# Kernel tuning notes

Hardware: AMD Instinct MI355X
Metric: run time of the kernel (lower is better)

The kernel has to match this reference:

```python
import jax, jax.numpy as jnp
import numpy as np

D, H, W, C = 24, 24, 16, 2        # image_dims + num_classes
THETA_ALPHA = 160.0               # bilateral spatial std
THETA_BETA = 3.0                  # bilateral intensity std
THETA_GAMMA = 3.0                 # spatial-only std
NUM_ITERATIONS = 5
N = D * H * W


def _gauss_kernel(feats):
    # Dense Gaussian kernel K_ij = exp(-0.5 * ||f_i - f_j||^2).
    # This is the exact filter that the permutohedral lattice approximates
    # (self-term included, matching the lattice splat/blur/slice behaviour).
    sq = jnp.sum(feats * feats, axis=-1)               # [N]
    d2 = sq[:, None] + sq[None, :] - 2.0 * feats @ feats.T
    return jnp.exp(-0.5 * jnp.maximum(d2, 0.0))        # [N, N]


def _positions():
    zz, yy, xx = jnp.meshgrid(jnp.arange(D), jnp.arange(H), jnp.arange(W), indexing='ij')
    return jnp.stack([zz, yy, xx], axis=-1).reshape(N, 3).astype(jnp.float32)


def setup_inputs() -> dict:
    key = jax.random.key(0)
    k1, k2 = jax.random.split(key)
    unaries = jax.random.normal(k1, (1, D, H, W, C), dtype=jnp.float32)
    rgb = jax.random.uniform(k2, (1, D, H, W, 1), dtype=jnp.float32)
    # learned params (build() initial values)
    spatial_ker_weights = jnp.array([1.41, 1.41], dtype=jnp.float32)
    bilateral_ker_weights = jnp.array([3.85, 3.85], dtype=jnp.float32)
    compatibility_matrix = jnp.eye(C, dtype=jnp.float32)
    return dict(unaries=unaries, rgb=rgb,
                spatial_ker_weights=spatial_ker_weights,
                bilateral_ker_weights=bilateral_ker_weights,
                compatibility_matrix=compatibility_matrix)


def reference(unaries, rgb, spatial_ker_weights, bilateral_ker_weights, compatibility_matrix):
    out_shape = unaries.shape
    u = unaries.reshape(N, C)                 # batch index 0 only, as in the TF code
    img = rgb.reshape(N, -1)
    pos = _positions()

    Ks = _gauss_kernel(pos / THETA_GAMMA)                                        # spatial kernel [N,N]
    Kb = _gauss_kernel(jnp.concatenate([pos / THETA_ALPHA, img / THETA_BETA], -1))  # bilateral kernel [N,N]

    # normalization = filter applied to all-ones (row sums)
    norm_s = jnp.sum(Ks, axis=-1, keepdims=True)   # [N,1]
    norm_b = jnp.sum(Kb, axis=-1, keepdims=True)   # [N,1]

    q = u
    for _ in range(NUM_ITERATIONS):
        spatial_out = (Ks @ q) / norm_s            # [N,C]
        bilateral_out = (Kb @ q) / norm_b          # [N,C]
        # diag(w_s) @ spatial.T + diag(w_b) @ bilateral.T  ==  per-class scaling
        message = spatial_out * spatial_ker_weights + bilateral_out * bilateral_ker_weights
        pairwise = message @ compatibility_matrix.T  # (compat @ msg.T).T
        q = u - pairwise
    return q.reshape(out_shape)
```

## Files before the change

### kernel.cpp

```cpp
#include <hip/hip_runtime.h>


#define DD 24
#define HH 24
#define WW 16
#define SLICE 384
#define NPTS 9216
#define NT 5
#define NFI 12
#define NFT 17
#define LOG2E 1.4426950408889634f
#define K3L   (LOG2E / 18.0f)
#define K160L (LOG2E / 51200.0f)

static __device__ __forceinline__ int iabs(int a) { return a < 0 ? -a : a; }

__global__ __launch_bounds__(SLICE)
void k_pre(const float2* __restrict__ u2, const float* __restrict__ rgb,
           float* __restrict__ tmp) {
    __shared__ float gk[32];
    __shared__ float sA[HH][WW + 1];
    __shared__ float sB[HH][WW + 1];
    const int z = blockIdx.x, f = blockIdx.y, t = threadIdx.x;
    const int y = t >> 4, x = t & 15;
    const int i = z * SLICE + t;

    const float kk = (f < 2) ? K3L : K160L;
    if (t < DD) gk[t] = exp2f(-(float)(t * t) * kk);

    float v;
    if (f < 2) {
        float2 q = u2[i];
        v = (f == 0) ? q.x : q.y;
    } else {
        float I3 = rgb[i] * (1.f / 3.f);
        float E = exp2f(-0.5f * LOG2E * I3 * I3);
        int k = (f < NFI) ? ((f - 2) >> 1) : (f - NFI);
        float P = E;
        for (int s = 0; s < k; ++s) P *= I3;
        if (f < NFI) {
            float2 q = u2[i];
            v = P * (((f - 2) & 1) ? q.y : q.x);
        } else {
            v = P;
        }
    }
    sA[y][x] = v;
    __syncthreads();

    float a = 0.f;
#pragma unroll
    for (int xp = 0; xp < WW; ++xp) a = fmaf(gk[iabs(x - xp)], sA[y][xp], a);
    sB[y][x] = a;
    __syncthreads();

    float b = 0.f;
#pragma unroll
    for (int yp = 0; yp < HH; ++yp) b = fmaf(gk[iabs(y - yp)], sB[yp][x], b);
    tmp[f * NPTS + i] = b;
}

__global__ __launch_bounds__(SLICE)
void k_zconv(const float* __restrict__ tmp, float* __restrict__ zout) {
    __shared__ float gk[32];
    const int z = blockIdx.x, f = blockIdx.y, t = threadIdx.x;
    const float kk = (f < 2) ? K3L : K160L;
    if (t < DD) gk[t] = exp2f(-(float)(t * t) * kk);
    __syncthreads();

    float acc = 0.f;
    const float* p = tmp + f * NPTS + t;
#pragma unroll 4
    for (int zp = 0; zp < DD; ++zp)
        acc = fmaf(gk[iabs(z - zp)], p[zp * SLICE], acc);
    zout[f * NPTS + z * SLICE + t] = acc;
}

static __device__ __forceinline__ void mf_update(
        const float acc[12], const float* g3s, const float* Pt,
        float inv_nb, int y, int x, int z,
        const float* sw, const float* bw, const float* compat,
        const float2 uu, float* q0o, float* q1o) {
    const float invf[NT] = {1.f, 1.f, 0.5f, 1.f / 6.f, 1.f / 24.f};
    float sx = 0.f, sy = 0.f, sz = 0.f;
#pragma unroll
    for (int xp = 0; xp < WW; ++xp) sx += g3s[iabs(x - xp)];
#pragma unroll
    for (int yp = 0; yp < HH; ++yp) sy += g3s[iabs(y - yp)];
#pragma unroll
    for (int zp = 0; zp < DD; ++zp) sz += g3s[iabs(z - zp)];
    const float inv_ns = 1.0f / (sx * sy * sz);

    float b0 = 0.f, b1 = 0.f;
#pragma unroll
    for (int k = 0; k < NT; ++k) {
        float w = Pt[k] * invf[k];
        b0 = fmaf(w, acc[2 + 2 * k], b0);
        b1 = fmaf(w, acc[3 + 2 * k], b1);
    }
    b0 *= inv_nb;
    b1 *= inv_nb;
    float s0 = acc[0] * inv_ns;
    float s1 = acc[1] * inv_ns;
    float m0 = s0 * sw[0] + b0 * bw[0];
    float m1 = s1 * sw[1] + b1 * bw[1];
    float p0 = fmaf(compat[0], m0, compat[1] * m1);
    float p1 = fmaf(compat[2], m0, compat[3] * m1);
    *q0o = uu.x - p0;
    *q1o = uu.y - p1;
}

__global__ __launch_bounds__(SLICE)
void k_xyupd(const float* __restrict__ zout, const float* __restrict__ rgb,
             const float2* __restrict__ u2,
             const float* __restrict__ sw, const float* __restrict__ bw,
             const float* __restrict__ compat,
             float* __restrict__ normb, float* __restrict__ tmp, int it) {
    __shared__ float g3s[32];
    __shared__ float gk[32];
    __shared__ float sA[HH][WW + 1];
    __shared__ float sB[HH][WW + 1];
    const int z = blockIdx.x, f = blockIdx.y, t = threadIdx.x;
    const int y = t >> 4, x = t & 15;
    const int i = z * SLICE + t;

    if (t < DD) {
        g3s[t] = exp2f(-(float)(t * t) * K3L);
        gk[t] = exp2f(-(float)(t * t) * ((f < 2) ? K3L : K160L));
    }
    __syncthreads();

    float acc[12];
#pragma unroll
    for (int k = 0; k < 12; ++k) acc[k] = zout[k * NPTS + i];

    const float I3 = rgb[i] * (1.f / 3.f);
    const float E = exp2f(-0.5f * LOG2E * I3 * I3);
    float Pt[NT];
    Pt[0] = E;
#pragma unroll
    for (int k = 1; k < NT; ++k) Pt[k] = Pt[k - 1] * I3;

    float inv_nb;
    if (it == 0) {
        const float invf[NT] = {1.f, 1.f, 0.5f, 1.f / 6.f, 1.f / 24.f};
        float nb = 0.f;
#pragma unroll
        for (int k = 0; k < NT; ++k)
            nb = fmaf(Pt[k] * invf[k], zout[(NFI + k) * NPTS + i], nb);
        if (f == 0) normb[i] = nb;
        inv_nb = 1.0f / nb;
    } else {
        inv_nb = 1.0f / normb[i];
    }

    float q0, q1;
    mf_update(acc, g3s, Pt, inv_nb, y, x, z, sw, bw, compat, u2[i], &q0, &q1);

    float v;
    if (f == 0) v = q0;
    else if (f == 1) v = q1;
    else {
        int k = (f - 2) >> 1;
        v = Pt[k] * (((f - 2) & 1) ? q1 : q0);
    }

    sA[y][x] = v;
    __syncthreads();
    float a = 0.f;
#pragma unroll
    for (int xp = 0; xp < WW; ++xp) a = fmaf(gk[iabs(x - xp)], sA[y][xp], a);
    sB[y][x] = a;
    __syncthreads();
    float b = 0.f;
#pragma unroll
    for (int yp = 0; yp < HH; ++yp) b = fmaf(gk[iabs(y - yp)], sB[yp][x], b);
    tmp[f * NPTS + i] = b;
}

__global__ __launch_bounds__(256)
void k_final(const float* __restrict__ zout, const float* __restrict__ rgb,
             const float2* __restrict__ u2,
             const float* __restrict__ sw, const float* __restrict__ bw,
             const float* __restrict__ compat,
             const float* __restrict__ normb, float2* __restrict__ out) {
    __shared__ float g3s[32];
    const int t = threadIdx.x;
    const int i = blockIdx.x * 256 + t;
    if (t < DD) g3s[t] = exp2f(-(float)(t * t) * K3L);
    __syncthreads();

    const int z = i / SLICE;
    const int yx = i - z * SLICE;
    const int y = yx >> 4, x = yx & 15;

    float acc[12];
#pragma unroll
    for (int k = 0; k < 12; ++k) acc[k] = zout[k * NPTS + i];

    const float I3 = rgb[i] * (1.f / 3.f);
    const float E = exp2f(-0.5f * LOG2E * I3 * I3);
    float Pt[NT];
    Pt[0] = E;
#pragma unroll
    for (int k = 1; k < NT; ++k) Pt[k] = Pt[k - 1] * I3;

    float q0, q1;
    mf_update(acc, g3s, Pt, 1.0f / normb[i], y, x, z, sw, bw, compat,
              u2[i], &q0, &q1);
    out[i] = make_float2(q0, q1);
}

extern "C" void kernel_launch(void* const* d_in, const int* in_sizes, int n_in,
                              void* d_out, int out_size, void* d_ws, size_t ws_size,
                              hipStream_t stream) {
    const float2* u2     = (const float2*)d_in[0];
    const float*  rgb    = (const float*)d_in[1];
    const float*  sw     = (const float*)d_in[2];
    const float*  bw     = (const float*)d_in[3];
    const float*  compat = (const float*)d_in[4];
    float2* out = (float2*)d_out;

    float* ws = (float*)d_ws;
    float* tmp   = ws;
    float* zout  = ws + NFT * NPTS;
    float* normb = ws + 2 * NFT * NPTS;

    k_pre<<<dim3(DD, NFT), SLICE, 0, stream>>>(u2, rgb, tmp);

    for (int it = 0; it < 5; ++it) {
        k_zconv<<<dim3(DD, it == 0 ? NFT : NFI), SLICE, 0, stream>>>(tmp, zout);
        if (it < 4)
            k_xyupd<<<dim3(DD, NFI), SLICE, 0, stream>>>(zout, rgb, u2, sw, bw,
                                                         compat, normb, tmp, it);
        else
            k_final<<<NPTS / 256, 256, 0, stream>>>(zout, rgb, u2, sw, bw,
                                                    compat, normb, out);
    }
}
```

Measured before the change: 103.8 us.

## Pack feature channels into float2 pairs and precompute spatial normalization

New measurement: 97.28 us (median of 2 runs). 6.3% less time.

```diff
diff --git a/kernel.cpp b/kernel.cpp
--- a/kernel.cpp
+++ b/kernel.cpp
@@ -7,101 +7,113 @@
 #define SLICE 384
 #define NPTS 9216
 #define NT 5
-#define NFI 12
-#define NFT 17
+#define NPAIR 6
+#define NPTOT 9
 #define LOG2E 1.4426950408889634f
 #define K3L   (LOG2E / 18.0f)
 #define K160L (LOG2E / 51200.0f)
+#define EXP2  __builtin_amdgcn_exp2f
 
 static __device__ __forceinline__ int iabs(int a) { return a < 0 ? -a : a; }
 
 __global__ __launch_bounds__(SLICE)
 void k_pre(const float2* __restrict__ u2, const float* __restrict__ rgb,
-           float* __restrict__ tmp) {
+           float2* __restrict__ tmp2, float* __restrict__ normS) {
     __shared__ float gk[32];
-    __shared__ float sA[HH][WW + 1];
-    __shared__ float sB[HH][WW + 1];
-    const int z = blockIdx.x, f = blockIdx.y, t = threadIdx.x;
+    __shared__ float2 sA[HH][WW + 1];
+    __shared__ float2 sB[HH][WW + 1];
+    const int z = blockIdx.x, p = blockIdx.y, t = threadIdx.x;
     const int y = t >> 4, x = t & 15;
     const int i = z * SLICE + t;
 
-    const float kk = (f < 2) ? K3L : K160L;
-    if (t < DD) gk[t] = exp2f(-(float)(t * t) * kk);
-
-    float v;
-    if (f < 2) {
+    const float kk = (p == 0) ? K3L : K160L;
+    if (t < DD) gk[t] = EXP2(-(float)(t * t) * kk);
+
+    const float I3 = rgb[i] * (1.f / 3.f);
+    float Pt[NT];
+    Pt[0] = EXP2(-0.5f * LOG2E * I3 * I3);
+#pragma unroll
+    for (int k = 1; k < NT; ++k) Pt[k] = Pt[k - 1] * I3;
+
+    float2 v;
+    if (p == 0) {
+        v = u2[i];
+    } else if (p < NPAIR) {
         float2 q = u2[i];
-        v = (f == 0) ? q.x : q.y;
+        float P = Pt[p - 1];
+        v = make_float2(P * q.x, P * q.y);
     } else {
-        float I3 = rgb[i] * (1.f / 3.f);
-        float E = exp2f(-0.5f * LOG2E * I3 * I3);
-        int k = (f < NFI) ? ((f - 2) >> 1) : (f - NFI);
-        float P = E;
-        for (int s = 0; s < k; ++s) P *= I3;
-        if (f < NFI) {
-            float2 q = u2[i];
-            v = P * (((f - 2) & 1) ? q.y : q.x);
-        } else {
-            v = P;
-        }
+        int j = p - NPAIR;
+        v = make_float2(Pt[2 * j], (j < 2) ? Pt[2 * j + 1] : 0.f);
     }
     sA[y][x] = v;
     __syncthreads();
 
-    float a = 0.f;
-#pragma unroll
-    for (int xp = 0; xp < WW; ++xp) a = fmaf(gk[iabs(x - xp)], sA[y][xp], a);
-    sB[y][x] = a;
-    __syncthreads();
-
-    float b = 0.f;
-#pragma unroll
-    for (int yp = 0; yp < HH; ++yp) b = fmaf(gk[iabs(y - yp)], sB[yp][x], b);
-    tmp[f * NPTS + i] = b;
+    float a0 = 0.f, a1 = 0.f;
+#pragma unroll
+    for (int xp = 0; xp < WW; ++xp) {
+        float w = gk[iabs(x - xp)];
+        float2 vv = sA[y][xp];
+        a0 = fmaf(w, vv.x, a0);
+        a1 = fmaf(w, vv.y, a1);
+    }
+    sB[y][x] = make_float2(a0, a1);
+    __syncthreads();
+    float b0 = 0.f, b1 = 0.f;
+#pragma unroll
+    for (int yp = 0; yp < HH; ++yp) {
+        float w = gk[iabs(y - yp)];
+        float2 vv = sB[yp][x];
+        b0 = fmaf(w, vv.x, b0);
+        b1 = fmaf(w, vv.y, b1);
+    }
+    tmp2[p * NPTS + i] = make_float2(b0, b1);
+
+    if (p == 0) {
+        float sx = 0.f, sy = 0.f, sz = 0.f;
+#pragma unroll
+        for (int xp = 0; xp < WW; ++xp) sx += gk[iabs(x - xp)];
+#pragma unroll
+        for (int yp = 0; yp < HH; ++yp) sy += gk[iabs(y - yp)];
+#pragma unroll
+        for (int zp = 0; zp < DD; ++zp) sz += gk[iabs(z - zp)];
+        normS[i] = 1.0f / (sx * sy * sz);
+    }
 }
 
 __global__ __launch_bounds__(SLICE)
-void k_zconv(const float* __restrict__ tmp, float* __restrict__ zout) {
-    __shared__ float gk[32];
-    const int z = blockIdx.x, f = blockIdx.y, t = threadIdx.x;
-    const float kk = (f < 2) ? K3L : K160L;
-    if (t < DD) gk[t] = exp2f(-(float)(t * t) * kk);
-    __syncthreads();
-
-    float acc = 0.f;
-    const float* p = tmp + f * NPTS + t;
-#pragma unroll 4
-    for (int zp = 0; zp < DD; ++zp)
-        acc = fmaf(gk[iabs(z - zp)], p[zp * SLICE], acc);
-    zout[f * NPTS + z * SLICE + t] = acc;
+void k_zconv(const float2* __restrict__ tmp2, float2* __restrict__ zout2) {
+    const int z = blockIdx.x, p = blockIdx.y, t = threadIdx.x;
+    const float kk = (p == 0) ? K3L : K160L;
+    float acc0 = 0.f, acc1 = 0.f;
+    const float2* src = tmp2 + p * NPTS + t;
+#pragma unroll 6
+    for (int zp = 0; zp < DD; ++zp) {
+        int d = z - zp;
+        float w = EXP2(-(float)(d * d) * kk);
+        float2 v = src[zp * SLICE];
+        acc0 = fmaf(w, v.x, acc0);
+        acc1 = fmaf(w, v.y, acc1);
+    }
+    zout2[p * NPTS + z * SLICE + t] = make_float2(acc0, acc1);
 }
 
 static __device__ __forceinline__ void mf_update(
-        const float acc[12], const float* g3s, const float* Pt,
-        float inv_nb, int y, int x, int z,
+        const float2 zp_[NPAIR], const float* Pt, float inv_ns, float inv_nb,
         const float* sw, const float* bw, const float* compat,
         const float2 uu, float* q0o, float* q1o) {
     const float invf[NT] = {1.f, 1.f, 0.5f, 1.f / 6.f, 1.f / 24.f};
-    float sx = 0.f, sy = 0.f, sz = 0.f;
-#pragma unroll
-    for (int xp = 0; xp < WW; ++xp) sx += g3s[iabs(x - xp)];
-#pragma unroll
-    for (int yp = 0; yp < HH; ++yp) sy += g3s[iabs(y - yp)];
-#pragma unroll
-    for (int zp = 0; zp < DD; ++zp) sz += g3s[iabs(z - zp)];
-    const float inv_ns = 1.0f / (sx * sy * sz);
-
     float b0 = 0.f, b1 = 0.f;
 #pragma unroll
     for (int k = 0; k < NT; ++k) {
         float w = Pt[k] * invf[k];
-        b0 = fmaf(w, acc[2 + 2 * k], b0);
-        b1 = fmaf(w, acc[3 + 2 * k], b1);
+        b0 = fmaf(w, zp_[1 + k].x, b0);
+        b1 = fmaf(w, zp_[1 + k].y, b1);
     }
     b0 *= inv_nb;
     b1 *= inv_nb;
-    float s0 = acc[0] * inv_ns;
-    float s1 = acc[1] * inv_ns;
+    float s0 = zp_[0].x * inv_ns;
+    float s1 = zp_[0].y * inv_ns;
     float m0 = s0 * sw[0] + b0 * bw[0];
     float m1 = s1 * sw[1] + b1 * bw[1];
     float p0 = fmaf(compat[0], m0, compat[1] * m1);
@@ -111,102 +123,96 @@
 }
 
 __global__ __launch_bounds__(SLICE)
-void k_xyupd(const float* __restrict__ zout, const float* __restrict__ rgb,
+void k_xyupd(const float2* __restrict__ zout2, const float* __restrict__ rgb,
              const float2* __restrict__ u2,
              const float* __restrict__ sw, const float* __restrict__ bw,
              const float* __restrict__ compat,
-             float* __restrict__ normb, float* __restrict__ tmp, int it) {
-    __shared__ float g3s[32];
+             const float* __restrict__ normS, float* __restrict__ normB,
+             float2* __restrict__ tmp2, int it) {
     __shared__ float gk[32];
-    __shared__ float sA[HH][WW + 1];
-    __shared__ float sB[HH][WW + 1];
-    const int z = blockIdx.x, f = blockIdx.y, t = threadIdx.x;
+    __shared__ float2 sA[HH][WW + 1];
+    __shared__ float2 sB[HH][WW + 1];
+    const int z = blockIdx.x, p = blockIdx.y, t = threadIdx.x;
     const int y = t >> 4, x = t & 15;
     const int i = z * SLICE + t;
 
-    if (t < DD) {
-        g3s[t] = exp2f(-(float)(t * t) * K3L);
-        gk[t] = exp2f(-(float)(t * t) * ((f < 2) ? K3L : K160L));
-    }
-    __syncthreads();
-
-    float acc[12];
-#pragma unroll
-    for (int k = 0; k < 12; ++k) acc[k] = zout[k * NPTS + i];
+    const float kk = (p == 0) ? K3L : K160L;
+    if (t < DD) gk[t] = EXP2(-(float)(t * t) * kk);
+
+    float2 zp_[NPAIR];
+#pragma unroll
+    for (int k = 0; k < NPAIR; ++k) zp_[k] = zout2[k * NPTS + i];
 
     const float I3 = rgb[i] * (1.f / 3.f);
-    const float E = exp2f(-0.5f * LOG2E * I3 * I3);
     float Pt[NT];
-    Pt[0] = E;
+    Pt[0] = EXP2(-0.5f * LOG2E * I3 * I3);
 #pragma unroll
     for (int k = 1; k < NT; ++k) Pt[k] = Pt[k - 1] * I3;
 
     float inv_nb;
     if (it == 0) {
-        const float invf[NT] = {1.f, 1.f, 0.5f, 1.f / 6.f, 1.f / 24.f};
-        float nb = 0.f;
-#pragma unroll
-        for (int k = 0; k < NT; ++k)
-            nb = fmaf(Pt[k] * invf[k], zout[(NFI + k) * NPTS + i], nb);
-        if (f == 0) normb[i] = nb;
+        float2 n0 = zout2[6 * NPTS + i];
+        float2 n1 = zout2[7 * NPTS + i];
+        float2 n2 = zout2[8 * NPTS + i];
+        float nb = Pt[0] * n0.x + Pt[1] * n0.y + 0.5f * Pt[2] * n1.x
+                 + (1.f / 6.f) * Pt[3] * n1.y + (1.f / 24.f) * Pt[4] * n2.x;
+        if (p == 0) normB[i] = nb;
         inv_nb = 1.0f / nb;
     } else {
-        inv_nb = 1.0f / normb[i];
+        inv_nb = 1.0f / normB[i];
     }
 
     float q0, q1;
-    mf_update(acc, g3s, Pt, inv_nb, y, x, z, sw, bw, compat, u2[i], &q0, &q1);
-
-    float v;
-    if (f == 0) v = q0;
-    else if (f == 1) v = q1;
-    else {
-        int k = (f - 2) >> 1;
-        v = Pt[k] * (((f - 2) & 1) ? q1 : q0);
-    }
+    mf_update(zp_, Pt, normS[i], inv_nb, sw, bw, compat, u2[i], &q0, &q1);
+
+    float2 v;
+    if (p == 0) v = make_float2(q0, q1);
+    else { float P = Pt[p - 1]; v = make_float2(P * q0, P * q1); }
 
     sA[y][x] = v;
     __syncthreads();
-    float a = 0.f;
-#pragma unroll
-    for (int xp = 0; xp < WW; ++xp) a = fmaf(gk[iabs(x - xp)], sA[y][xp], a);
-    sB[y][x] = a;
-    __syncthreads();
-    float b = 0.f;
-#pragma unroll
-    for (int yp = 0; yp < HH; ++yp) b = fmaf(gk[iabs(y - yp)], sB[yp][x], b);
-    tmp[f * NPTS + i] = b;
+    float a0 = 0.f, a1 = 0.f;
+#pragma unroll
+    for (int xp = 0; xp < WW; ++xp) {
+        float w = gk[iabs(x - xp)];
+        float2 vv = sA[y][xp];
+        a0 = fmaf(w, vv.x, a0);
+        a1 = fmaf(w, vv.y, a1);
+    }
+    sB[y][x] = make_float2(a0, a1);
+    __syncthreads();
+    float b0 = 0.f, b1 = 0.f;
+#pragma unroll
+    for (int yp = 0; yp < HH; ++yp) {
+        float w = gk[iabs(y - yp)];
+        float2 vv = sB[yp][x];
+        b0 = fmaf(w, vv.x, b0);
+        b1 = fmaf(w, vv.y, b1);
+    }
+    tmp2[p * NPTS + i] = make_float2(b0, b1);
 }
 
 __global__ __launch_bounds__(256)
-void k_final(const float* __restrict__ zout, const float* __restrict__ rgb,
+void k_final(const float2* __restrict__ zout2, const float* __restrict__ rgb,
              const float2* __restrict__ u2,
              const float* __restrict__ sw, const float* __restrict__ bw,
              const float* __restrict__ compat,
-             const float* __restrict__ normb, float2* __restrict__ out) {
-    __shared__ float g3s[32];
-    const int t = threadIdx.x;
-    const int i = blockIdx.x * 256 + t;
-    if (t < DD) g3s[t] = exp2f(-(float)(t * t) * K3L);
-    __syncthreads();
-
-    const int z = i / SLICE;
-    const int yx = i - z * SLICE;
-    const int y = yx >> 4, x = yx & 15;
-
-    float acc[12];
-#pragma unroll
-    for (int k = 0; k < 12; ++k) acc[k] = zout[k * NPTS + i];
+             const float* __restrict__ normS, const float* __restrict__ normB,
+             float2* __restrict__ out) {
+    const int i = blockIdx.x * 256 + threadIdx.x;
+
+    float2 zp_[NPAIR];
+#pragma unroll
+    for (int k = 0; k < NPAIR; ++k) zp_[k] = zout2[k * NPTS + i];
 
     const float I3 = rgb[i] * (1.f / 3.f);
-    const float E = exp2f(-0.5f * LOG2E * I3 * I3);
     float Pt[NT];
-    Pt[0] = E;
+    Pt[0] = EXP2(-0.5f * LOG2E * I3 * I3);
 #pragma unroll
     for (int k = 1; k < NT; ++k) Pt[k] = Pt[k - 1] * I3;
 
     float q0, q1;
-    mf_update(acc, g3s, Pt, 1.0f / normb[i], y, x, z, sw, bw, compat,
+    mf_update(zp_, Pt, normS[i], 1.0f / normB[i], sw, bw, compat,
               u2[i], &q0, &q1);
     out[i] = make_float2(q0, q1);
 }
@@ -221,20 +227,22 @@
     const float*  compat = (const float*)d_in[4];
     float2* out = (float2*)d_out;
 
-    float* ws = (float*)d_ws;
-    float* tmp   = ws;
-    float* zout  = ws + NFT * NPTS;
-    float* normb = ws + 2 * NFT * NPTS;
-
-    k_pre<<<dim3(DD, NFT), SLICE, 0, stream>>>(u2, rgb, tmp);
+    float2* ws2   = (float2*)d_ws;
+    float2* tmp2  = ws2;
+    float2* zout2 = ws2 + NPTOT * NPTS;
+    float*  normS = (float*)(ws2 + 2 * NPTOT * NPTS);
+    float*  normB = normS + NPTS;
+
+    k_pre<<<dim3(DD, NPTOT), SLICE, 0, stream>>>(u2, rgb, tmp2, normS);
 
     for (int it = 0; it < 5; ++it) {
-        k_zconv<<<dim3(DD, it == 0 ? NFT : NFI), SLICE, 0, stream>>>(tmp, zout);
+        k_zconv<<<dim3(DD, it == 0 ? NPTOT : NPAIR), SLICE, 0, stream>>>(tmp2, zout2);
         if (it < 4)
-            k_xyupd<<<dim3(DD, NFI), SLICE, 0, stream>>>(zout, rgb, u2, sw, bw,
-                                                         compat, normb, tmp, it);
+            k_xyupd<<<dim3(DD, NPAIR), SLICE, 0, stream>>>(zout2, rgb, u2, sw, bw,
+                                                           compat, normS, normB,
+                                                           tmp2, it);
         else
-            k_final<<<NPTS / 256, 256, 0, stream>>>(zout, rgb, u2, sw, bw,
-                                                    compat, normb, out);
-    }
-}
+            k_final<<<NPTS / 256, 256, 0, stream>>>(zout2, rgb, u2, sw, bw,
+                                                    compat, normS, normB, out);
+    }
+}
```
